# Kernel tuning notes

Hardware: AMD Instinct MI355X
Metric: run time of the kernel (lower is better)

Reference implementation:

```python
import jax, jax.numpy as jnp
import numpy as np

EMBED_DIM = 1024
ATTN_DIM = 1024


def setup_inputs() -> dict:
    key = jax.random.key(0)
    k1, k2, k3, k4 = jax.random.split(key, 4)
    scale = 1.0 / np.sqrt(EMBED_DIM)
    return {
        "embedded": jax.random.normal(k1, (4, 2048, EMBED_DIM), dtype=jnp.float32),
        # weights stored as [in, out] (torch Linear applies x @ W.T)
        "Wk": jax.random.uniform(k2, (EMBED_DIM, ATTN_DIM), dtype=jnp.float32, minval=-scale, maxval=scale),
        "Wq": jax.random.uniform(k3, (EMBED_DIM, ATTN_DIM), dtype=jnp.float32, minval=-scale, maxval=scale),
        "Wv": jax.random.uniform(k4, (EMBED_DIM, ATTN_DIM), dtype=jnp.float32, minval=-scale, maxval=scale),
    }


def reference(embedded, Wk, Wq, Wv):
    b, t, _ = embedded.shape
    k = embedded @ Wk  # [b, t, d]
    q = embedded @ Wq
    v = embedded @ Wv
    scores = jnp.einsum("btd,bsd->bts", q, k) / jnp.sqrt(jnp.float32(k.shape[-1]))
    causal = jnp.tril(jnp.ones((t, t), dtype=bool))  # [t, t]
    scores = jnp.where(causal, scores, -jnp.inf)
    w = jax.nn.softmax(scores, axis=-1)
    o = jnp.einsum("bts,bsd->btd", w, v)
    return jnp.round(o * 10000.0) / 10000.0
```

## Files before the change

kernel.cpp:

```cpp
#include <hip/hip_runtime.h>
#include <cmath>

typedef _Float16 half8 __attribute__((ext_vector_type(8)));
typedef _Float16 half4 __attribute__((ext_vector_type(4)));
typedef float floatx4 __attribute__((ext_vector_type(4)));

__device__ __forceinline__ void load_lds16(const void* g, void* l) {
  __builtin_amdgcn_global_load_lds((const __attribute__((address_space(1))) void*)g,
                                   (__attribute__((address_space(3))) void*)l, 16, 0, 0);
}


__global__ void prep_kernel(const float* __restrict__ emb, const float* __restrict__ Wq,
                            const float* __restrict__ Wk, const float* __restrict__ Wv,
                            _Float16* __restrict__ Xp, _Float16* __restrict__ Wqp,
                            _Float16* __restrict__ Wkp, _Float16* __restrict__ Wvtp) {
  int p = blockIdx.x;
  if (p < 640) {
    __shared__ _Float16 lds[16 * 1032];
    const float* src;
    _Float16* dst;
    if (p < 512)      { src = emb + (size_t)p * 16384;        dst = Xp  + (size_t)p * 16384; }
    else if (p < 576) { src = Wq + (size_t)(p - 512) * 16384; dst = Wqp + (size_t)(p - 512) * 16384; }
    else              { src = Wk + (size_t)(p - 576) * 16384; dst = Wkp + (size_t)(p - 576) * 16384; }
    for (int it = 0; it < 16; ++it) {
      int idx = it * 256 + threadIdx.x;
      int row = idx >> 8, c4 = idx & 255;
      float4 v = ((const float4*)src)[row * 256 + c4];
      half4 h;
      h[0] = (_Float16)v.x; h[1] = (_Float16)v.y; h[2] = (_Float16)v.z; h[3] = (_Float16)v.w;
      *(half4*)(lds + row * 1032 + c4 * 4) = h;
    }
    __syncthreads();
    for (int it = 0; it < 8; ++it) {
      int c = it * 256 + threadIdx.x;
      int kb = c >> 6, k16 = (c >> 4) & 3, r = c & 15;
      half8 h = *(const half8*)(lds + r * 1032 + kb * 32 + k16 * 8);
      *(half8*)(dst + (size_t)c * 8) = h;
    }
  } else {
    __shared__ float tile[32][33];
    int q = p - 640;
    int n0 = (q & 31) * 32, k0 = (q >> 5) * 32;
    int c = threadIdx.x & 31, r8 = threadIdx.x >> 5;
    for (int pp = 0; pp < 4; ++pp) {
      int r = pp * 8 + r8;
      tile[r][c] = Wv[(size_t)(k0 + r) * 1024 + n0 + c];
    }
    __syncthreads();
    if (threadIdx.x < 128) {
      int rr = threadIdx.x & 31;
      int k16 = (threadIdx.x >> 5) & 3;
      half8 h;
      for (int kk = 0; kk < 8; ++kk) h[kk] = (_Float16)tile[k16 * 8 + kk][rr];
      int n_row = n0 + rr;
      size_t chunk = ((size_t)(n_row >> 4) * 32 + (k0 >> 5)) * 64 + (k16 << 4) + (n_row & 15);
      *(half8*)(Wvtp + chunk * 8) = h;
    }
  }
}

__device__ __forceinline__ void gemm_core(const _Float16* __restrict__ Ap, int kbA, int tA0,
                                          const _Float16* __restrict__ Bp, int kbB, int tB0,
                                          int kIters, _Float16* sA, _Float16* sB,
                                          floatx4 acc[4][4]) {
  int tid = threadIdx.x;
  int lane = tid & 63, wave = tid >> 6;
  int wm = (wave >> 1) << 6, wn = (wave & 1) << 6;
  const _Float16* gA0 = Ap + ((size_t)(tA0 + 2 * wave) * kbA) * 512 + lane * 8;
  const _Float16* gA1 = Ap + ((size_t)(tA0 + 2 * wave + 1) * kbA) * 512 + lane * 8;
  const _Float16* gB0 = Bp + ((size_t)(tB0 + 2 * wave) * kbB) * 512 + lane * 8;
  const _Float16* gB1 = Bp + ((size_t)(tB0 + 2 * wave + 1) * kbB) * 512 + lane * 8;
  int ta = wm >> 4, tb = wn >> 4, lo = lane * 8;
  int wo = wave * 1024;

  load_lds16(gA0, sA + wo);
  load_lds16(gA1, sA + wo + 512);
  load_lds16(gB0, sB + wo);
  load_lds16(gB1, sB + wo + 512);
  __syncthreads();

  int cur = 0;
  for (int kt = 0; kt < kIters; ++kt) {
    if (kt + 1 < kIters) {
      size_t kb = (size_t)(kt + 1) * 512;
      int nx = (cur ^ 1) << 12;
      load_lds16(gA0 + kb, sA + nx + wo);
      load_lds16(gA1 + kb, sA + nx + wo + 512);
      load_lds16(gB0 + kb, sB + nx + wo);
      load_lds16(gB1 + kb, sB + nx + wo + 512);
    }
    const _Float16* cA = sA + (cur << 12);
    const _Float16* cB = sB + (cur << 12);
    half8 af[4], bf[4];
    for (int i = 0; i < 4; ++i) af[i] = *(const half8*)(cA + (ta + i) * 512 + lo);
    for (int j = 0; j < 4; ++j) bf[j] = *(const half8*)(cB + (tb + j) * 512 + lo);
    __builtin_amdgcn_s_setprio(1);
    for (int i = 0; i < 4; ++i)
      for (int j = 0; j < 4; ++j)
        acc[i][j] = __builtin_amdgcn_mfma_f32_16x16x32_f16(af[i], bf[j], acc[i][j], 0, 0, 0);
    __builtin_amdgcn_s_setprio(0);
    if (kt + 1 < kIters) {
      __syncthreads();
      cur ^= 1;
    }
  }
}

__global__ void mt_kernel(const _Float16* __restrict__ Wkp, const _Float16* __restrict__ Wqp,
                          _Float16* __restrict__ Mtp) {
  __shared__ __align__(16) _Float16 sA[8192];
  __shared__ __align__(16) _Float16 sB[8192];
  floatx4 acc[4][4];
  for (int i = 0; i < 4; ++i)
    for (int j = 0; j < 4; ++j) acc[i][j] = (floatx4){0.f, 0.f, 0.f, 0.f};
  int m0 = blockIdx.y * 128, n0 = blockIdx.x * 128;
  gemm_core(Wkp, 32, m0 >> 4, Wqp, 32, n0 >> 4, 32, sA, sB, acc);
  int lane = threadIdx.x & 63, wave = threadIdx.x >> 6;
  int wm = (wave >> 1) << 6, wn = (wave & 1) << 6;
  int quad = lane >> 4, cl = lane & 15;
  for (int i = 0; i < 4; ++i)
    for (int j = 0; j < 4; ++j)
      for (int rr = 0; rr < 4; ++rr) {
        int row = m0 + wm + i * 16 + quad * 4 + rr;
        int col = n0 + wn + j * 16 + cl;
        size_t chunk = ((size_t)(row >> 4) * 32 + (col >> 5)) * 64 + (((col >> 3) & 3) << 4) + (row & 15);
        Mtp[chunk * 8 + (col & 7)] = (_Float16)acc[i][j][rr];
      }
}

__global__ void proj_kernel(const _Float16* __restrict__ Xp, const _Float16* __restrict__ Bp,
                            _Float16* __restrict__ XMp, _Float16* __restrict__ Vtp) {
  __shared__ __align__(16) _Float16 sA[8192];
  __shared__ __align__(16) _Float16 sB[8192];
  floatx4 acc[4][4];
  for (int i = 0; i < 4; ++i)
    for (int j = 0; j < 4; ++j) acc[i][j] = (floatx4){0.f, 0.f, 0.f, 0.f};
  int orig = blockIdx.y * 16 + blockIdx.x;
  int tile = (orig & 7) * 128 + (orig >> 3);
  int m0 = (tile >> 4) * 128, n0 = (tile & 15) * 128;
  gemm_core(Xp, 32, m0 >> 4, Bp, 32, n0 >> 4, 32, sA, sB, acc);
  int lane = threadIdx.x & 63, wave = threadIdx.x >> 6;
  int wm = (wave >> 1) << 6, wn = (wave & 1) << 6;
  int quad = lane >> 4, cl = lane & 15;
  int which = n0 >> 10;
  int colbase = (n0 & 1023) + wn;
  for (int i = 0; i < 4; ++i)
    for (int j = 0; j < 4; ++j)
      for (int rr = 0; rr < 4; ++rr) {
        int row_g = m0 + wm + i * 16 + quad * 4 + rr;
        int col = colbase + j * 16 + cl;
        _Float16 val = (_Float16)acc[i][j][rr];
        int b = row_g >> 11, t = row_g & 2047;
        if (which == 1) {
          size_t chunk = ((size_t)(col >> 4) * 64 + (t >> 5)) * 64 + (((t >> 3) & 3) << 4) + (col & 15);
          Vtp[(size_t)b * 2097152 + chunk * 8 + (t & 7)] = val;
        } else {
          size_t chunk = ((size_t)(t >> 4) * 32 + (col >> 5)) * 64 + (((col >> 3) & 3) << 4) + (t & 15);
          XMp[(size_t)b * 2097152 + chunk * 8 + (col & 7)] = val;
        }
      }
}

__global__ void qke_kernel(const _Float16* __restrict__ XMp, const _Float16* __restrict__ Xp,
                           _Float16* __restrict__ E, float* __restrict__ lsum) {
  __shared__ __align__(16) _Float16 sA[8192];
  __shared__ __align__(16) _Float16 sB[8192];
  int x = blockIdx.x, b = blockIdx.y;
  int p = (x & 7) * 17 + (x >> 3);
  int ti = 0;
  while ((ti + 1) * (ti + 2) / 2 <= p) ++ti;
  int tj = p - ti * (ti + 1) / 2;
  const _Float16* Ab = XMp + (size_t)b * 2097152;
  const _Float16* Bb = Xp + (size_t)b * 2097152;
  _Float16* Eb = E + (size_t)b * 4194304;
  floatx4 acc[4][4];
  for (int i = 0; i < 4; ++i)
    for (int j = 0; j < 4; ++j) acc[i][j] = (floatx4){0.f, 0.f, 0.f, 0.f};
  gemm_core(Ab, 32, ti * 8, Bb, 32, tj * 8, 32, sA, sB, acc);
  int lane = threadIdx.x & 63, wave = threadIdx.x >> 6;
  int wm = (wave >> 1) << 6, wn = (wave & 1) << 6;
  int quad = lane >> 4, cl = lane & 15;
  float rs[4][4];
  for (int i = 0; i < 4; ++i)
    for (int rr = 0; rr < 4; ++rr) rs[i][rr] = 0.f;
  for (int i = 0; i < 4; ++i)
    for (int j = 0; j < 4; ++j)
      for (int rr = 0; rr < 4; ++rr) {
        int row = ti * 128 + wm + i * 16 + quad * 4 + rr;
        int col = tj * 128 + wn + j * 16 + cl;
        float e = 0.f;
        if (col <= row) e = __expf(acc[i][j][rr] * 0.03125f - 12.0f);
        _Float16 eh = (_Float16)e;
        rs[i][rr] += (float)eh;
        size_t chunk = ((size_t)(row >> 4) * 64 + (col >> 5)) * 64 + (((col >> 3) & 3) << 4) + (row & 15);
        Eb[chunk * 8 + (col & 7)] = eh;
      }
  float* lb = lsum + (size_t)b * 2048;
  for (int i = 0; i < 4; ++i)
    for (int rr = 0; rr < 4; ++rr) {
      float v = rs[i][rr];
      v += __shfl_xor(v, 1, 64);
      v += __shfl_xor(v, 2, 64);
      v += __shfl_xor(v, 4, 64);
      v += __shfl_xor(v, 8, 64);
      if (cl == 0) atomicAdd(lb + ti * 128 + wm + i * 16 + quad * 4 + rr, v);
    }
}

__global__ void pv_kernel(const _Float16* __restrict__ E, const _Float16* __restrict__ Vtp,
                          const float* __restrict__ lsum, float* __restrict__ out) {
  __shared__ __align__(16) _Float16 sA[8192];
  __shared__ __align__(16) _Float16 sB[8192];
  int orig = blockIdx.x + 8 * (blockIdx.y + 16 * blockIdx.z);
  int logical = (orig & 7) * 64 + (orig >> 3);
  int n0 = (logical & 7) * 128;
  int rest = logical >> 3;
  int y = rest & 15, b = rest >> 4;
  int ti = (y & 1) ? (15 - (y >> 1)) : (y >> 1);
  const _Float16* Pb = E + (size_t)b * 4194304;
  const _Float16* Vb = Vtp + (size_t)b * 2097152;
  floatx4 acc[4][4];
  for (int i = 0; i < 4; ++i)
    for (int j = 0; j < 4; ++j) acc[i][j] = (floatx4){0.f, 0.f, 0.f, 0.f};
  gemm_core(Pb, 64, ti * 8, Vb, 64, n0 >> 4, (ti + 1) * 4, sA, sB, acc);
  int lane = threadIdx.x & 63, wave = threadIdx.x >> 6;
  int wm = (wave >> 1) << 6, wn = (wave & 1) << 6;
  int quad = lane >> 4, cl = lane & 15;
  const float* lb = lsum + (size_t)b * 2048;
  for (int i = 0; i < 4; ++i)
    for (int rr = 0; rr < 4; ++rr) {
      int row = ti * 128 + wm + i * 16 + quad * 4 + rr;
      float inv = 1.0f / lb[row];
      for (int j = 0; j < 4; ++j) {
        int col = n0 + wn + j * 16 + cl;
        float v = acc[i][j][rr] * inv;
        out[((size_t)b * 2048 + row) * 1024 + col] = rintf(v * 10000.f) * 1e-4f;
      }
    }
}

extern "C" void kernel_launch(void* const* d_in, const int* in_sizes, int n_in,
                              void* d_out, int out_size, void* d_ws, size_t ws_size,
                              hipStream_t stream) {
  const float* emb = (const float*)d_in[0];
  const float* Wk = (const float*)d_in[1];
  const float* Wq = (const float*)d_in[2];
  const float* Wv = (const float*)d_in[3];
  float* out = (float*)d_out;

  _Float16* ws = (_Float16*)d_ws;
  _Float16* Xp   = ws;
  _Float16* Wqp  = Xp + (size_t)8192 * 1024;
  _Float16* Wkp  = Wqp + (size_t)1024 * 1024;
  _Float16* Mtp  = Wkp + (size_t)1024 * 1024;
  _Float16* Wvtp = Mtp + (size_t)1024 * 1024;
  _Float16* XMp  = Wvtp + (size_t)1024 * 1024;
  _Float16* Vtp  = XMp + (size_t)8192 * 1024;
  _Float16* Ebuf = Vtp + (size_t)8192 * 1024;
  float* lsum    = (float*)(Ebuf + (size_t)16 * 1024 * 1024);

  hipMemsetAsync(lsum, 0, 4 * 2048 * sizeof(float), stream);
  prep_kernel<<<1664, 256, 0, stream>>>(emb, Wq, Wk, Wv, Xp, Wqp, Wkp, Wvtp);
  mt_kernel<<<dim3(8, 8), 256, 0, stream>>>(Wkp, Wqp, Mtp);
  proj_kernel<<<dim3(16, 64), 256, 0, stream>>>(Xp, Mtp, XMp, Vtp);
  qke_kernel<<<dim3(136, 4), 256, 0, stream>>>(XMp, Xp, Ebuf, lsum);
  pv_kernel<<<dim3(8, 16, 4), 256, 0, stream>>>(Ebuf, Vtp, lsum, out);
}
```

Measured before the change: 235.0 us.

## Replace projection GEMM with 256x256-tile, 8-wave double-buffered pipelined kernel

The projection GEMM (X times [M|Wv^T]) now uses 256x256 output tiles with 512 threads, a 128 KB double-buffered LDS tile and direct global-to-LDS loads. Loads for the next K-steps are interleaved with MFMA phases under explicit vmcnt waits, barriers and setprio. The larger tiles are meant to raise arithmetic intensity and hide memory latency. The cost is only 256 blocks, one per CU, and heavy register and LDS pressure.

New measurement: 233.5 us. No clear change (-0.6%).

```diff
diff --git a/kernel.cpp b/kernel.cpp
--- a/kernel.cpp
+++ b/kernel.cpp
@@ -129,35 +129,117 @@
       }
 }
 
-__global__ void proj_kernel(const _Float16* __restrict__ Xp, const _Float16* __restrict__ Bp,
-                            _Float16* __restrict__ XMp, _Float16* __restrict__ Vtp) {
-  __shared__ __align__(16) _Float16 sA[8192];
-  __shared__ __align__(16) _Float16 sB[8192];
-  floatx4 acc[4][4];
-  for (int i = 0; i < 4; ++i)
-    for (int j = 0; j < 4; ++j) acc[i][j] = (floatx4){0.f, 0.f, 0.f, 0.f};
-  int orig = blockIdx.y * 16 + blockIdx.x;
-  int tile = (orig & 7) * 128 + (orig >> 3);
-  int m0 = (tile >> 4) * 128, n0 = (tile & 15) * 128;
-  gemm_core(Xp, 32, m0 >> 4, Bp, 32, n0 >> 4, 32, sA, sB, acc);
-  int lane = threadIdx.x & 63, wave = threadIdx.x >> 6;
-  int wm = (wave >> 1) << 6, wn = (wave & 1) << 6;
+#define NT_PROJ 16
+
+__global__ __launch_bounds__(512, 2) void proj256_kernel(
+    const _Float16* __restrict__ Ap, const _Float16* __restrict__ Bp,
+    _Float16* __restrict__ XMp, _Float16* __restrict__ Vtp) {
+  __shared__ __align__(16) _Float16 sh[65536];
+  int tid = threadIdx.x;
+  int lane = tid & 63, w = tid >> 6;
+  int wr = w >> 2, wc = w & 3;
+  int orig = blockIdx.x;
+  int tile = (orig & 7) * 32 + (orig >> 3);
+  int mtile = tile >> 3, ntile = tile & 7;
+  int tA0 = mtile * 16, tB0 = ntile * 16;
+
+  const _Float16* gB[4];
+  int ldsB[4];
+  for (int i = 0; i < 4; ++i) {
+    int cb = w * 4 + i, pc = cb >> 1, kb = cb & 1;
+    gB[i] = Bp + ((size_t)(tB0 + pc) * 32 + kb) * 512 + lane * 8;
+    ldsB[i] = 16384 + cb * 512;
+  }
+  const _Float16* gA[4];
+  int ldsA[4];
+  {
+    int kbw = w & 1, pihi = (w >> 2) * 8, pilo = (w >> 1) & 1;
+    for (int q = 0; q < 4; ++q) {
+      int p = 2 * q + pilo + pihi;
+      gA[q] = Ap + ((size_t)(tA0 + p) * 32 + kbw) * 512 + lane * 8;
+      ldsA[q] = (p * 2 + kbw) * 512;
+    }
+  }
+
+  floatx4 acc[8][4];
+  for (int m = 0; m < 8; ++m)
+    for (int n = 0; n < 4; ++n) acc[m][n] = (floatx4){0.f, 0.f, 0.f, 0.f};
+
+  for (int tt = 0; tt < 2; ++tt) {
+    int bo = tt << 15;
+    for (int i = 0; i < 4; ++i) load_lds16(gB[i] + (size_t)tt * 1024, sh + bo + ldsB[i]);
+    for (int q = 0; q < 4; ++q) load_lds16(gA[q] + (size_t)tt * 1024, sh + bo + ldsA[q]);
+  }
+  asm volatile("s_waitcnt vmcnt(8)" ::: "memory");
+  __builtin_amdgcn_s_barrier();
+
+  half8 bf[4][2];
+#pragma unroll 2
+  for (int t = 0; t < NT_PROJ; ++t) {
+    int bo = (t & 1) << 15;
+    const _Float16* base = sh + bo;
+#pragma unroll
+    for (int q = 0; q < 4; ++q) {
+      half8 af[2][2];
+      if (q == 0) {
+        for (int n = 0; n < 4; ++n)
+          for (int kb = 0; kb < 2; ++kb)
+            bf[n][kb] = *(const half8*)(base + 16384 + ((wc * 4 + n) * 2 + kb) * 512 + lane * 8);
+      }
+      for (int mm = 0; mm < 2; ++mm)
+        for (int kb = 0; kb < 2; ++kb)
+          af[mm][kb] = *(const half8*)(base + ((wr * 8 + 2 * q + mm) * 2 + kb) * 512 + lane * 8);
+      if (q == 0) {
+        if (t >= 1 && t + 1 < NT_PROJ)
+          load_lds16(gA[3] + (size_t)(t + 1) * 1024, sh + (bo ^ 32768) + ldsA[3]);
+      } else if (q == 1) {
+        if (t + 2 < NT_PROJ)
+          for (int i = 0; i < 4; ++i)
+            load_lds16(gB[i] + (size_t)(t + 2) * 1024, sh + bo + ldsB[i]);
+      } else if (q == 2) {
+        if (t + 2 < NT_PROJ) {
+          load_lds16(gA[0] + (size_t)(t + 2) * 1024, sh + bo + ldsA[0]);
+          load_lds16(gA[1] + (size_t)(t + 2) * 1024, sh + bo + ldsA[1]);
+        }
+      } else {
+        if (t < NT_PROJ - 1) {
+          if (t + 2 < NT_PROJ) asm volatile("s_waitcnt vmcnt(6)" ::: "memory");
+          else                 asm volatile("s_waitcnt vmcnt(0)" ::: "memory");
+        }
+        if (t + 2 < NT_PROJ)
+          load_lds16(gA[2] + (size_t)(t + 2) * 1024, sh + bo + ldsA[2]);
+      }
+      asm volatile("" ::: "memory");
+      __builtin_amdgcn_s_barrier();
+      asm volatile("s_waitcnt lgkmcnt(0)" ::: "memory");
+      __builtin_amdgcn_sched_barrier(0);
+      __builtin_amdgcn_s_setprio(1);
+      for (int mm = 0; mm < 2; ++mm)
+        for (int n = 0; n < 4; ++n)
+          for (int kb = 0; kb < 2; ++kb)
+            acc[2 * q + mm][n] =
+                __builtin_amdgcn_mfma_f32_16x16x32_f16(af[mm][kb], bf[n][kb], acc[2 * q + mm][n], 0, 0, 0);
+      __builtin_amdgcn_s_setprio(0);
+      asm volatile("" ::: "memory");
+      __builtin_amdgcn_s_barrier();
+    }
+  }
+
   int quad = lane >> 4, cl = lane & 15;
-  int which = n0 >> 10;
-  int colbase = (n0 & 1023) + wn;
-  for (int i = 0; i < 4; ++i)
-    for (int j = 0; j < 4; ++j)
+  int which = ntile >> 2;
+  for (int m = 0; m < 8; ++m)
+    for (int n = 0; n < 4; ++n)
       for (int rr = 0; rr < 4; ++rr) {
-        int row_g = m0 + wm + i * 16 + quad * 4 + rr;
-        int col = colbase + j * 16 + cl;
-        _Float16 val = (_Float16)acc[i][j][rr];
-        int b = row_g >> 11, t = row_g & 2047;
-        if (which == 1) {
-          size_t chunk = ((size_t)(col >> 4) * 64 + (t >> 5)) * 64 + (((t >> 3) & 3) << 4) + (col & 15);
-          Vtp[(size_t)b * 2097152 + chunk * 8 + (t & 7)] = val;
+        int row_g = mtile * 256 + wr * 128 + m * 16 + quad * 4 + rr;
+        int colg = (ntile & 3) * 256 + wc * 64 + n * 16 + cl;
+        _Float16 val = (_Float16)acc[m][n][rr];
+        int b = row_g >> 11, tt = row_g & 2047;
+        if (which) {
+          size_t chunk = ((size_t)(colg >> 4) * 64 + (tt >> 5)) * 64 + (((tt >> 3) & 3) << 4) + (colg & 15);
+          Vtp[(size_t)b * 2097152 + chunk * 8 + (tt & 7)] = val;
         } else {
-          size_t chunk = ((size_t)(t >> 4) * 32 + (col >> 5)) * 64 + (((col >> 3) & 3) << 4) + (t & 15);
-          XMp[(size_t)b * 2097152 + chunk * 8 + (col & 7)] = val;
+          size_t chunk = ((size_t)(tt >> 4) * 32 + (colg >> 5)) * 64 + (((colg >> 3) & 3) << 4) + (tt & 15);
+          XMp[(size_t)b * 2097152 + chunk * 8 + (colg & 7)] = val;
         }
       }
 }
@@ -263,7 +345,7 @@
   hipMemsetAsync(lsum, 0, 4 * 2048 * sizeof(float), stream);
   prep_kernel<<<1664, 256, 0, stream>>>(emb, Wq, Wk, Wv, Xp, Wqp, Wkp, Wvtp);
   mt_kernel<<<dim3(8, 8), 256, 0, stream>>>(Wkp, Wqp, Mtp);
-  proj_kernel<<<dim3(16, 64), 256, 0, stream>>>(Xp, Mtp, XMp, Vtp);
+  proj256_kernel<<<256, 512, 0, stream>>>(Xp, Mtp, XMp, Vtp);
   qke_kernel<<<dim3(136, 4), 256, 0, stream>>>(XMp, Xp, Ebuf, lsum);
   pv_kernel<<<dim3(8, 16, 4), 256, 0, stream>>>(Ebuf, Vtp, lsum, out);
 }
```
